# Kernel tuning notes

Measured on AMD Instinct MI355X. Metric: run time of the kernel, lower is better.

Reference implementation:

```python
import jax, jax.numpy as jnp
import numpy as np

EMBED = 256
HEADS = 8
LEVELS = 1
POINTS = 4
NBQ = 2          # num_bev_queue
HBEV = 128
WBEV = 128
BS = 1


def setup_inputs() -> dict:
    key = jax.random.key(0)
    ks = jax.random.split(key, 10)
    Nq = HBEV * WBEV
    E = EMBED
    so_out = NBQ * HEADS * LEVELS * POINTS * 2
    aw_out = NBQ * HEADS * LEVELS * POINTS
    return {
        "query": jax.random.normal(ks[0], (BS, Nq, E), jnp.float32),
        "value": jax.random.normal(ks[1], (BS, NBQ * Nq, E), jnp.float32),
        "reference_points": jax.random.uniform(ks[2], (BS, Nq, LEVELS, 2), jnp.float32),
        # params stored as [in, out]; y = x @ W + b (math-equivalent to torch Linear)
        "W_vproj": jax.random.normal(ks[3], (E, E), jnp.float32) / np.sqrt(E).astype(np.float32),
        "b_vproj": jnp.zeros((E,), jnp.float32),
        "W_so": jax.random.normal(ks[4], (NBQ * E, so_out), jnp.float32) * 0.01,
        "b_so": jax.random.normal(ks[5], (so_out,), jnp.float32) * 0.5,
        "W_aw": jax.random.normal(ks[6], (NBQ * E, aw_out), jnp.float32) * 0.01,
        "b_aw": jnp.zeros((aw_out,), jnp.float32),
        "W_out": jax.random.normal(ks[7], (E, E), jnp.float32) / np.sqrt(E).astype(np.float32),
        "b_out": jnp.zeros((E,), jnp.float32),
        "spatial_shapes": jnp.array([[HBEV, WBEV]], jnp.int32),
        "level_start_index": jnp.array([0], jnp.int32),
    }


def _msda(value, spatial_shapes, sampling_locations, attention_weights):
    """Multi-scale deformable attention (grid_sample semantics: bilinear,
    zero padding, align_corners=False).
    value: [B, sum(H*W), Hh, d]; sampling_locations: [B, Nq, Hh, L, P, 2] in [0,1];
    attention_weights: [B, Nq, Hh, L, P]. Returns [B, Nq, Hh*d]."""
    B, _, Hh, d = value.shape
    _, Nq, _, L, P, _ = sampling_locations.shape
    ss = np.asarray(spatial_shapes)
    out = jnp.zeros((B, Nq, Hh, d), value.dtype)
    start = 0
    for l in range(L):
        H_, W_ = int(ss[l, 0]), int(ss[l, 1])
        v = value[:, start:start + H_ * W_]          # [B, H*W, Hh, d]
        start += H_ * W_
        loc = sampling_locations[:, :, :, l]          # [B, Nq, Hh, P, 2]
        # align_corners=False: pixel = loc*size - 0.5
        px = loc[..., 0] * W_ - 0.5
        py = loc[..., 1] * H_ - 0.5
        x0f = jnp.floor(px)
        y0f = jnp.floor(py)
        lx = px - x0f
        ly = py - y0f
        x0 = x0f.astype(jnp.int32)
        y0 = y0f.astype(jnp.int32)

        def gather(ix, iy):
            valid = ((ix >= 0) & (ix < W_) & (iy >= 0) & (iy < H_))
            idx = jnp.clip(iy, 0, H_ - 1) * W_ + jnp.clip(ix, 0, W_ - 1)   # [B,Nq,Hh,P]
            idx = jnp.transpose(idx, (0, 1, 3, 2)).reshape(B, Nq * P, Hh, 1)
            g = jnp.take_along_axis(v, idx, axis=1).reshape(B, Nq, P, Hh, d)
            m = jnp.transpose(valid, (0, 1, 3, 2))[..., None].astype(value.dtype)
            return g * m

        def wmul(w):  # [B,Nq,Hh,P] -> [B,Nq,P,Hh,1]
            return jnp.transpose(w, (0, 1, 3, 2))[..., None]

        sampled = (wmul((1 - lx) * (1 - ly)) * gather(x0, y0)
                   + wmul(lx * (1 - ly)) * gather(x0 + 1, y0)
                   + wmul((1 - lx) * ly) * gather(x0, y0 + 1)
                   + wmul(lx * ly) * gather(x0 + 1, y0 + 1))   # [B,Nq,P,Hh,d]
        out = out + jnp.einsum('bqphd,bqhp->bqhd', sampled, attention_weights[:, :, :, l])
    return out.reshape(B, Nq, Hh * d)


def reference(query, value, reference_points, W_vproj, b_vproj, W_so, b_so,
              W_aw, b_aw, W_out, b_out, spatial_shapes, level_start_index):
    bs, Nq, E = query.shape
    Hh, L, P, nbq = HEADS, LEVELS, POINTS, NBQ
    identity = query
    # query enhanced with the previous-BEV slice of value
    qe = jnp.concatenate([value[:, :Nq], query], axis=-1)        # [bs, Nq, 2E]
    v = (value @ W_vproj + b_vproj).reshape(bs * nbq, Nq, Hh, E // Hh)
    so = (qe @ W_so + b_so).reshape(bs, Nq, Hh, nbq, L, P, 2)
    aw = jax.nn.softmax((qe @ W_aw + b_aw).reshape(bs, Nq, Hh, nbq, L * P), axis=-1)
    aw = aw.reshape(bs, Nq, Hh, nbq, L, P)
    aw = jnp.transpose(aw, (0, 3, 1, 2, 4, 5)).reshape(bs * nbq, Nq, Hh, L, P)
    so = jnp.transpose(so, (0, 3, 1, 2, 4, 5, 6)).reshape(bs * nbq, Nq, Hh, L, P, 2)
    rp = jnp.tile(reference_points, (nbq, 1, 1, 1))              # [bs*nbq, Nq, L, 2]
    ssf = spatial_shapes.astype(so.dtype)
    offset_normalizer = jnp.stack([ssf[:, 1], ssf[:, 0]], -1)    # [L, 2] = (W, H)
    loc = rp[:, :, None, :, None, :] + so / offset_normalizer[None, None, None, :, None, :]
    out = _msda(v, spatial_shapes, loc, aw).reshape(bs, nbq, Nq, E).mean(axis=1)
    out = out @ W_out + b_out
    return out + identity  # dropout is identity in eval mode
```

## Files before the change

kernel.cpp:

```cpp
#include <hip/hip_runtime.h>
#include <math.h>

#define NQ     16384
#define NHEAD  8
#define GW     128
#define GH     128

typedef __attribute__((ext_vector_type(8))) short short8;
typedef __attribute__((ext_vector_type(4))) float f32x4;

static __device__ __forceinline__ unsigned short f2bf(float f) {
    unsigned u = __builtin_bit_cast(unsigned, f);
    u += 0x7FFFu + ((u >> 16) & 1u);
    return (unsigned short)(u >> 16);
}
static __device__ __forceinline__ unsigned pk2(float lo, float hi) {
    return (unsigned)f2bf(lo) | ((unsigned)f2bf(hi) << 16);
}
static __device__ __forceinline__ float bflo(unsigned u) {
    return __builtin_bit_cast(float, u << 16);
}
static __device__ __forceinline__ float bfhi(unsigned u) {
    return __builtin_bit_cast(float, u & 0xffff0000u);
}

__global__ void prep(const float* __restrict__ Wv, const float* __restrict__ Wso,
                     const float* __restrict__ Waw, const float* __restrict__ bso,
                     const float* __restrict__ baw, const float* __restrict__ Wo,
                     unsigned short* __restrict__ WTv, unsigned short* __restrict__ WTso,
                     unsigned short* __restrict__ WTo, float* __restrict__ bias2)
{
    const int n = blockIdx.x;
    const int k = threadIdx.x;
    WTv[n * 256 + k] = f2bf(Wv[(size_t)k * 256 + n]);
    WTo[n * 256 + k] = f2bf(Wo[(size_t)k * 256 + n]);
    float s0, s1;
    if (n < 128)      { s0 = Wso[(size_t)k * 128 + n];       s1 = Wso[(size_t)(k + 256) * 128 + n]; }
    else if (n < 192) { s0 = Waw[(size_t)k * 64 + n - 128];  s1 = Waw[(size_t)(k + 256) * 64 + n - 128]; }
    else              { s0 = 0.f; s1 = 0.f; }
    WTso[(size_t)n * 512 + k]       = f2bf(s0);
    WTso[(size_t)n * 512 + k + 256] = f2bf(s1);
    if (k == 0) bias2[n] = (n < 128) ? bso[n] : ((n < 192) ? baw[n - 128] : 0.f);
}

template<int KTOT, int MODE>
static __device__ __forceinline__ void gemm_body(
    int m0, int n0,
    const float* __restrict__ A1, const float* __restrict__ A2,
    const unsigned short* __restrict__ Abf,
    const unsigned short* __restrict__ WT,
    const float* __restrict__ bias, const float* __restrict__ resid,
    void* __restrict__ Cout,
    unsigned short* As, unsigned short* Bs)
{
    const int tid = threadIdx.x;
    const int w = tid >> 6, lane = tid & 63;
    const int wr = w >> 1, wc = w & 1;
    const int g = lane >> 4, r16 = lane & 15;

    f32x4 acc[4][4] = {};

    for (int k0 = 0; k0 < KTOT; k0 += 64) {
        if (MODE == 2) {
            #pragma unroll
            for (int c = 0; c < 4; ++c) {
                int idx = tid + c * 256;
                int row = idx >> 3, oct = idx & 7;
                uint4 wv = *reinterpret_cast<const uint4*>(
                    &Abf[(size_t)(m0 + row) * 256 + k0 + oct * 8]);
                *reinterpret_cast<uint4*>(&As[(oct * 128 + row) * 8]) = wv;
            }
        } else {
            const float* Asrc = (KTOT == 512 && k0 >= 256) ? (A2 + (k0 - 256)) : (A1 + k0);
            #pragma unroll
            for (int c = 0; c < 4; ++c) {
                int idx = tid + c * 256;
                int row = idx >> 3, oct = idx & 7;
                const float* p = Asrc + (size_t)(m0 + row) * 256 + oct * 8;
                float4 f0 = *reinterpret_cast<const float4*>(p);
                float4 f1 = *reinterpret_cast<const float4*>(p + 4);
                uint4 wv;
                wv.x = pk2(f0.x, f0.y); wv.y = pk2(f0.z, f0.w);
                wv.z = pk2(f1.x, f1.y); wv.w = pk2(f1.z, f1.w);
                *reinterpret_cast<uint4*>(&As[(oct * 128 + row) * 8]) = wv;
            }
        }
        #pragma unroll
        for (int c = 0; c < 4; ++c) {
            int idx = tid + c * 256;
            int n = idx >> 3, oct = idx & 7;
            uint4 wv = *reinterpret_cast<const uint4*>(
                &WT[(size_t)(n0 + n) * KTOT + k0 + oct * 8]);
            *reinterpret_cast<uint4*>(&Bs[(oct * 128 + n) * 8]) = wv;
        }
        __syncthreads();

        #pragma unroll
        for (int kh = 0; kh < 2; ++kh) {
            short8 af[4], bfr[4];
            #pragma unroll
            for (int m = 0; m < 4; ++m)
                af[m] = *reinterpret_cast<const short8*>(
                    &As[(((kh * 4 + g) * 128) + wr * 64 + m * 16 + r16) * 8]);
            #pragma unroll
            for (int n = 0; n < 4; ++n)
                bfr[n] = *reinterpret_cast<const short8*>(
                    &Bs[(((kh * 4 + g) * 128) + wc * 64 + n * 16 + r16) * 8]);
            #pragma unroll
            for (int m = 0; m < 4; ++m)
                #pragma unroll
                for (int n = 0; n < 4; ++n)
                    acc[m][n] = __builtin_amdgcn_mfma_f32_16x16x32_bf16(
                        af[m], bfr[n], acc[m][n], 0, 0, 0);
        }
        __syncthreads();
    }

    #pragma unroll
    for (int m = 0; m < 4; ++m) {
        int row = m0 + wr * 64 + m * 16 + g * 4;
        #pragma unroll
        for (int n = 0; n < 4; ++n) {
            int col = n0 + wc * 64 + n * 16 + r16;
            if (MODE == 1 && col >= 192) continue;
            float bia = bias[col];
            #pragma unroll
            for (int j = 0; j < 4; ++j) {
                float vo = acc[m][n][j] + bia;
                if (MODE == 0) {
                    ((unsigned short*)Cout)[(size_t)(row + j) * 256 + col] = f2bf(vo);
                } else if (MODE == 1) {
                    ((float*)Cout)[(size_t)(row + j) * 192 + col] = vo;
                } else {
                    ((float*)Cout)[(size_t)(row + j) * 256 + col] =
                        vo + resid[(size_t)(row + j) * 256 + col];
                }
            }
        }
    }
}

__global__ __launch_bounds__(256, 2)
void gemm_vs(const float* __restrict__ value, const float* __restrict__ query,
             const unsigned short* __restrict__ WTv, const unsigned short* __restrict__ WTso,
             const float* __restrict__ bv, const float* __restrict__ bias2,
             unsigned short* __restrict__ v_out, float* __restrict__ soaw_out)
{
    __shared__ __align__(16) unsigned short As[8 * 128 * 8];
    __shared__ __align__(16) unsigned short Bs[8 * 128 * 8];
    const int bid = blockIdx.x;
    if (bid < 512) {
        gemm_body<256, 0>((bid >> 1) * 128, (bid & 1) * 128,
                          value, nullptr, nullptr, WTv, bv, nullptr, v_out, As, Bs);
    } else {
        const int b2 = bid - 512;
        gemm_body<512, 1>((b2 >> 1) * 128, (b2 & 1) * 128,
                          value, query, nullptr, WTso, bias2, nullptr, soaw_out, As, Bs);
    }
}

__global__ __launch_bounds__(256, 2)
void gemm_out(const unsigned short* __restrict__ Abf, const unsigned short* __restrict__ WTo,
              const float* __restrict__ bo, const float* __restrict__ resid,
              float* __restrict__ out)
{
    __shared__ __align__(16) unsigned short As[8 * 128 * 8];
    __shared__ __align__(16) unsigned short Bs[8 * 128 * 8];
    const int bid = blockIdx.x;
    gemm_body<256, 2>((bid >> 1) * 128, (bid & 1) * 128,
                      nullptr, nullptr, Abf, WTo, bo, resid, out, As, Bs);
}

static __device__ __forceinline__ void acc8(float* acc, float w, uint4 r) {
    acc[0] = fmaf(w, bflo(r.x), acc[0]);
    acc[1] = fmaf(w, bfhi(r.x), acc[1]);
    acc[2] = fmaf(w, bflo(r.y), acc[2]);
    acc[3] = fmaf(w, bfhi(r.y), acc[3]);
    acc[4] = fmaf(w, bflo(r.z), acc[4]);
    acc[5] = fmaf(w, bfhi(r.z), acc[5]);
    acc[6] = fmaf(w, bflo(r.w), acc[6]);
    acc[7] = fmaf(w, bfhi(r.w), acc[7]);
}

__global__ __launch_bounds__(256)
void sampler(const unsigned short* __restrict__ v, const float* __restrict__ soaw,
             const float* __restrict__ rp, unsigned short* __restrict__ outm)
{
    __shared__ float so_s[8][128];
    __shared__ float w_s[8][64];
    __shared__ float rp_s[8][2];

    const int t = threadIdx.x;
    const int bid = blockIdx.x;
    const int q0 = ((bid & 7) * 256 + (bid >> 3)) * 8;

    #pragma unroll
    for (int i = 0; i < 4; ++i) {
        int idx = t + i * 256;
        int qq = idx >> 7, off = idx & 127;
        so_s[qq][off] = soaw[(size_t)(q0 + qq) * 192 + off];
    }
    if (t < 128) {
        int qq = t >> 4, grp = t & 15;
        float4 a4 = *reinterpret_cast<const float4*>(
            &soaw[(size_t)(q0 + qq) * 192 + 128 + grp * 4]);
        float m = fmaxf(fmaxf(a4.x, a4.y), fmaxf(a4.z, a4.w));
        float e0 = __expf(a4.x - m), e1 = __expf(a4.y - m);
        float e2 = __expf(a4.z - m), e3 = __expf(a4.w - m);
        float inv = 1.f / (e0 + e1 + e2 + e3);
        w_s[qq][grp * 4 + 0] = e0 * inv;
        w_s[qq][grp * 4 + 1] = e1 * inv;
        w_s[qq][grp * 4 + 2] = e2 * inv;
        w_s[qq][grp * 4 + 3] = e3 * inv;
    }
    if (t < 16) rp_s[t >> 1][t & 1] = rp[(size_t)(q0 + (t >> 1)) * 2 + (t & 1)];
    __syncthreads();

    const int wq = t >> 5;
    const int q = q0 + wq;
    const int s = t & 31;
    const int h = s >> 2, c = s & 3;
    const int sub = h * 64 + c * 16;
    const float rpx = rp_s[wq][0], rpy = rp_s[wq][1];
    float acc[8] = {};

    #pragma unroll
    for (int b = 0; b < 2; ++b) {
        const char* vb = (const char*)v + (size_t)b * NQ * 512;
        #pragma unroll
        for (int p = 0; p < 4; ++p) {
            float sox = so_s[wq][h * 16 + b * 8 + p * 2 + 0];
            float soy = so_s[wq][h * 16 + b * 8 + p * 2 + 1];
            float wbp = w_s[wq][h * 8 + b * 4 + p];
            float px = (rpx + sox * (1.0f / 128.0f)) * 128.0f - 0.5f;
            float py = (rpy + soy * (1.0f / 128.0f)) * 128.0f - 0.5f;
            float x0f = floorf(px), y0f = floorf(py);
            float lx = px - x0f, ly = py - y0f;
            int x0 = (int)x0f, y0 = (int)y0f;
            int x1 = x0 + 1, y1 = y0 + 1;
            float wx0 = (1.f - lx) * ((x0 >= 0 && x0 < GW) ? 1.f : 0.f);
            float wx1 = lx         * ((x1 >= 0 && x1 < GW) ? 1.f : 0.f);
            float wy0 = (1.f - ly) * ((y0 >= 0 && y0 < GH) ? 1.f : 0.f);
            float wy1 = ly         * ((y1 >= 0 && y1 < GH) ? 1.f : 0.f);
            int x0c = min(max(x0, 0), GW - 1), x1c = min(max(x1, 0), GW - 1);
            int y0c = min(max(y0, 0), GH - 1), y1c = min(max(y1, 0), GH - 1);
            uint4 r00 = *(const uint4*)(vb + ((size_t)(y0c * GW + x0c) * 512 + sub));
            uint4 r10 = *(const uint4*)(vb + ((size_t)(y0c * GW + x1c) * 512 + sub));
            uint4 r01 = *(const uint4*)(vb + ((size_t)(y1c * GW + x0c) * 512 + sub));
            uint4 r11 = *(const uint4*)(vb + ((size_t)(y1c * GW + x1c) * 512 + sub));
            acc8(acc, wbp * wx0 * wy0, r00);
            acc8(acc, wbp * wx1 * wy0, r10);
            acc8(acc, wbp * wx0 * wy1, r01);
            acc8(acc, wbp * wx1 * wy1, r11);
        }
    }

    uint4 o;
    o.x = pk2(0.5f * acc[0], 0.5f * acc[1]);
    o.y = pk2(0.5f * acc[2], 0.5f * acc[3]);
    o.z = pk2(0.5f * acc[4], 0.5f * acc[5]);
    o.w = pk2(0.5f * acc[6], 0.5f * acc[7]);
    *reinterpret_cast<uint4*>((char*)outm + (size_t)q * 512 + sub) = o;
}

extern "C" void kernel_launch(void* const* d_in, const int* in_sizes, int n_in,
                              void* d_out, int out_size, void* d_ws, size_t ws_size,
                              hipStream_t stream)
{
    const float* query   = (const float*)d_in[0];
    const float* value   = (const float*)d_in[1];
    const float* rp      = (const float*)d_in[2];
    const float* W_vproj = (const float*)d_in[3];
    const float* b_vproj = (const float*)d_in[4];
    const float* W_so    = (const float*)d_in[5];
    const float* b_so    = (const float*)d_in[6];
    const float* W_aw    = (const float*)d_in[7];
    const float* b_aw    = (const float*)d_in[8];
    const float* W_out   = (const float*)d_in[9];
    const float* b_out   = (const float*)d_in[10];
    float* out = (float*)d_out;

    char* wp = (char*)d_ws;
    unsigned short* ws_v    = (unsigned short*)wp; wp += (size_t)2 * NQ * 256 * 2;
    float*          ws_soaw = (float*)wp;          wp += (size_t)NQ * 192 * 4;
    unsigned short* ws_mean = (unsigned short*)wp; wp += (size_t)NQ * 256 * 2;
    unsigned short* WTv     = (unsigned short*)wp; wp += 256 * 256 * 2;
    unsigned short* WTso    = (unsigned short*)wp; wp += 256 * 512 * 2;
    unsigned short* WTo     = (unsigned short*)wp; wp += 256 * 256 * 2;
    float*          bias2   = (float*)wp;          wp += 256 * 4;

    prep<<<dim3(256), dim3(256), 0, stream>>>(W_vproj, W_so, W_aw, b_so, b_aw, W_out,
                                              WTv, WTso, WTo, bias2);
    gemm_vs<<<dim3(768), dim3(256), 0, stream>>>(value, query, WTv, WTso,
                                                 b_vproj, bias2, ws_v, ws_soaw);
    sampler<<<dim3(NQ / 8), dim3(256), 0, stream>>>(ws_v, ws_soaw, rp, ws_mean);
    gemm_out<<<dim3(256), dim3(256), 0, stream>>>(ws_mean, WTo, b_out, query, out);
}
```

Baseline: 95.53 us.

## Pad GEMM LDS tiles, remap block roles, split sampler queues across half-waves

The GEMM shared-memory tiles get a padded stride (1032 instead of 1024 per k-octet) to reduce LDS bank conflicts on the MFMA fragment loads. Block indices are remapped so consecutive blocks share row tiles differently, aiming at better cache locality. The sampler now uses a 64-lane wave per query, with each half-wave handling one BEV queue and combining results by a cross-lane shuffle. This doubles parallelism and the number of sampler blocks. It adds a shuffle and leaves half the lanes idle during the store.

```diff
diff --git a/kernel.cpp b/kernel.cpp
--- a/kernel.cpp
+++ b/kernel.cpp
@@ -43,6 +43,8 @@
     if (k == 0) bias2[n] = (n < 128) ? bso[n] : ((n < 192) ? baw[n - 128] : 0.f);
 }
 
+#define PL(oct, row) ((oct) * 1032 + (row) * 8)
+
 template<int KTOT, int MODE>
 static __device__ __forceinline__ void gemm_body(
     int m0, int n0,
@@ -68,7 +70,7 @@
                 int row = idx >> 3, oct = idx & 7;
                 uint4 wv = *reinterpret_cast<const uint4*>(
                     &Abf[(size_t)(m0 + row) * 256 + k0 + oct * 8]);
-                *reinterpret_cast<uint4*>(&As[(oct * 128 + row) * 8]) = wv;
+                *reinterpret_cast<uint4*>(&As[PL(oct, row)]) = wv;
             }
         } else {
             const float* Asrc = (KTOT == 512 && k0 >= 256) ? (A2 + (k0 - 256)) : (A1 + k0);
@@ -82,7 +84,7 @@
                 uint4 wv;
                 wv.x = pk2(f0.x, f0.y); wv.y = pk2(f0.z, f0.w);
                 wv.z = pk2(f1.x, f1.y); wv.w = pk2(f1.z, f1.w);
-                *reinterpret_cast<uint4*>(&As[(oct * 128 + row) * 8]) = wv;
+                *reinterpret_cast<uint4*>(&As[PL(oct, row)]) = wv;
             }
         }
         #pragma unroll
@@ -91,7 +93,7 @@
             int n = idx >> 3, oct = idx & 7;
             uint4 wv = *reinterpret_cast<const uint4*>(
                 &WT[(size_t)(n0 + n) * KTOT + k0 + oct * 8]);
-            *reinterpret_cast<uint4*>(&Bs[(oct * 128 + n) * 8]) = wv;
+            *reinterpret_cast<uint4*>(&Bs[PL(oct, n)]) = wv;
         }
         __syncthreads();
 
@@ -101,11 +103,11 @@
             #pragma unroll
             for (int m = 0; m < 4; ++m)
                 af[m] = *reinterpret_cast<const short8*>(
-                    &As[(((kh * 4 + g) * 128) + wr * 64 + m * 16 + r16) * 8]);
+                    &As[PL(kh * 4 + g, wr * 64 + m * 16 + r16)]);
             #pragma unroll
             for (int n = 0; n < 4; ++n)
                 bfr[n] = *reinterpret_cast<const short8*>(
-                    &Bs[(((kh * 4 + g) * 128) + wc * 64 + n * 16 + r16) * 8]);
+                    &Bs[PL(kh * 4 + g, wc * 64 + n * 16 + r16)]);
             #pragma unroll
             for (int m = 0; m < 4; ++m)
                 #pragma unroll
@@ -146,15 +148,17 @@
              const float* __restrict__ bv, const float* __restrict__ bias2,
              unsigned short* __restrict__ v_out, float* __restrict__ soaw_out)
 {
-    __shared__ __align__(16) unsigned short As[8 * 128 * 8];
-    __shared__ __align__(16) unsigned short Bs[8 * 128 * 8];
-    const int bid = blockIdx.x;
-    if (bid < 512) {
-        gemm_body<256, 0>((bid >> 1) * 128, (bid & 1) * 128,
+    __shared__ __align__(16) unsigned short As[8 * 1032];
+    __shared__ __align__(16) unsigned short Bs[8 * 1032];
+    const int b = blockIdx.x;
+    if (b < 512) {
+        const int role = ((b >> 4) * 8 + (b & 7)) * 2 + ((b >> 3) & 1);
+        gemm_body<256, 0>((role >> 1) * 128, (role & 1) * 128,
                           value, nullptr, nullptr, WTv, bv, nullptr, v_out, As, Bs);
     } else {
-        const int b2 = bid - 512;
-        gemm_body<512, 1>((b2 >> 1) * 128, (b2 & 1) * 128,
+        const int j = b - 512;
+        const int role = ((j >> 4) * 8 + (j & 7)) * 2 + ((j >> 3) & 1);
+        gemm_body<512, 1>((role >> 1) * 128, (role & 1) * 128,
                           value, query, nullptr, WTso, bias2, nullptr, soaw_out, As, Bs);
     }
 }
@@ -164,10 +168,11 @@
               const float* __restrict__ bo, const float* __restrict__ resid,
               float* __restrict__ out)
 {
-    __shared__ __align__(16) unsigned short As[8 * 128 * 8];
-    __shared__ __align__(16) unsigned short Bs[8 * 128 * 8];
-    const int bid = blockIdx.x;
-    gemm_body<256, 2>((bid >> 1) * 128, (bid & 1) * 128,
+    __shared__ __align__(16) unsigned short As[8 * 1032];
+    __shared__ __align__(16) unsigned short Bs[8 * 1032];
+    const int b = blockIdx.x;
+    const int role = ((b >> 4) * 8 + (b & 7)) * 2 + ((b >> 3) & 1);
+    gemm_body<256, 2>((role >> 1) * 128, (role & 1) * 128,
                       nullptr, nullptr, Abf, WTo, bo, resid, out, As, Bs);
 }
 
@@ -186,21 +191,21 @@
 void sampler(const unsigned short* __restrict__ v, const float* __restrict__ soaw,
              const float* __restrict__ rp, unsigned short* __restrict__ outm)
 {
-    __shared__ float so_s[8][128];
-    __shared__ float w_s[8][64];
-    __shared__ float rp_s[8][2];
+    __shared__ float so_s[4][128];
+    __shared__ float w_s[4][64];
+    __shared__ float rp_s[4][2];
 
     const int t = threadIdx.x;
     const int bid = blockIdx.x;
-    const int q0 = ((bid & 7) * 256 + (bid >> 3)) * 8;
+    const int q0 = ((bid & 7) * 512 + (bid >> 3)) * 4;
 
     #pragma unroll
-    for (int i = 0; i < 4; ++i) {
+    for (int i = 0; i < 2; ++i) {
         int idx = t + i * 256;
         int qq = idx >> 7, off = idx & 127;
         so_s[qq][off] = soaw[(size_t)(q0 + qq) * 192 + off];
     }
-    if (t < 128) {
+    if (t < 64) {
         int qq = t >> 4, grp = t & 15;
         float4 a4 = *reinterpret_cast<const float4*>(
             &soaw[(size_t)(q0 + qq) * 192 + 128 + grp * 4]);
@@ -213,54 +218,58 @@
         w_s[qq][grp * 4 + 2] = e2 * inv;
         w_s[qq][grp * 4 + 3] = e3 * inv;
     }
-    if (t < 16) rp_s[t >> 1][t & 1] = rp[(size_t)(q0 + (t >> 1)) * 2 + (t & 1)];
+    if (t < 8) rp_s[t >> 1][t & 1] = rp[(size_t)(q0 + (t >> 1)) * 2 + (t & 1)];
     __syncthreads();
 
-    const int wq = t >> 5;
+    const int wq = t >> 6;
     const int q = q0 + wq;
-    const int s = t & 31;
+    const int ln = t & 63;
+    const int b = ln >> 5;
+    const int s = ln & 31;
     const int h = s >> 2, c = s & 3;
     const int sub = h * 64 + c * 16;
     const float rpx = rp_s[wq][0], rpy = rp_s[wq][1];
+    const char* vb = (const char*)v + (size_t)b * NQ * 512;
     float acc[8] = {};
 
     #pragma unroll
-    for (int b = 0; b < 2; ++b) {
-        const char* vb = (const char*)v + (size_t)b * NQ * 512;
-        #pragma unroll
-        for (int p = 0; p < 4; ++p) {
-            float sox = so_s[wq][h * 16 + b * 8 + p * 2 + 0];
-            float soy = so_s[wq][h * 16 + b * 8 + p * 2 + 1];
-            float wbp = w_s[wq][h * 8 + b * 4 + p];
-            float px = (rpx + sox * (1.0f / 128.0f)) * 128.0f - 0.5f;
-            float py = (rpy + soy * (1.0f / 128.0f)) * 128.0f - 0.5f;
-            float x0f = floorf(px), y0f = floorf(py);
-            float lx = px - x0f, ly = py - y0f;
-            int x0 = (int)x0f, y0 = (int)y0f;
-            int x1 = x0 + 1, y1 = y0 + 1;
-            float wx0 = (1.f - lx) * ((x0 >= 0 && x0 < GW) ? 1.f : 0.f);
-            float wx1 = lx         * ((x1 >= 0 && x1 < GW) ? 1.f : 0.f);
-            float wy0 = (1.f - ly) * ((y0 >= 0 && y0 < GH) ? 1.f : 0.f);
-            float wy1 = ly         * ((y1 >= 0 && y1 < GH) ? 1.f : 0.f);
-            int x0c = min(max(x0, 0), GW - 1), x1c = min(max(x1, 0), GW - 1);
-            int y0c = min(max(y0, 0), GH - 1), y1c = min(max(y1, 0), GH - 1);
-            uint4 r00 = *(const uint4*)(vb + ((size_t)(y0c * GW + x0c) * 512 + sub));
-            uint4 r10 = *(const uint4*)(vb + ((size_t)(y0c * GW + x1c) * 512 + sub));
-            uint4 r01 = *(const uint4*)(vb + ((size_t)(y1c * GW + x0c) * 512 + sub));
-            uint4 r11 = *(const uint4*)(vb + ((size_t)(y1c * GW + x1c) * 512 + sub));
-            acc8(acc, wbp * wx0 * wy0, r00);
-            acc8(acc, wbp * wx1 * wy0, r10);
-            acc8(acc, wbp * wx0 * wy1, r01);
-            acc8(acc, wbp * wx1 * wy1, r11);
-        }
-    }
-
-    uint4 o;
-    o.x = pk2(0.5f * acc[0], 0.5f * acc[1]);
-    o.y = pk2(0.5f * acc[2], 0.5f * acc[3]);
-    o.z = pk2(0.5f * acc[4], 0.5f * acc[5]);
-    o.w = pk2(0.5f * acc[6], 0.5f * acc[7]);
-    *reinterpret_cast<uint4*>((char*)outm + (size_t)q * 512 + sub) = o;
+    for (int p = 0; p < 4; ++p) {
+        float sox = so_s[wq][h * 16 + b * 8 + p * 2 + 0];
+        float soy = so_s[wq][h * 16 + b * 8 + p * 2 + 1];
+        float wbp = w_s[wq][h * 8 + b * 4 + p];
+        float px = (rpx + sox * (1.0f / 128.0f)) * 128.0f - 0.5f;
+        float py = (rpy + soy * (1.0f / 128.0f)) * 128.0f - 0.5f;
+        float x0f = floorf(px), y0f = floorf(py);
+        float lx = px - x0f, ly = py - y0f;
+        int x0 = (int)x0f, y0 = (int)y0f;
+        int x1 = x0 + 1, y1 = y0 + 1;
+        float wx0 = (1.f - lx) * ((x0 >= 0 && x0 < GW) ? 1.f : 0.f);
+        float wx1 = lx         * ((x1 >= 0 && x1 < GW) ? 1.f : 0.f);
+        float wy0 = (1.f - ly) * ((y0 >= 0 && y0 < GH) ? 1.f : 0.f);
+        float wy1 = ly         * ((y1 >= 0 && y1 < GH) ? 1.f : 0.f);
+        int x0c = min(max(x0, 0), GW - 1), x1c = min(max(x1, 0), GW - 1);
+        int y0c = min(max(y0, 0), GH - 1), y1c = min(max(y1, 0), GH - 1);
+        uint4 r00 = *(const uint4*)(vb + ((size_t)(y0c * GW + x0c) * 512 + sub));
+        uint4 r10 = *(const uint4*)(vb + ((size_t)(y0c * GW + x1c) * 512 + sub));
+        uint4 r01 = *(const uint4*)(vb + ((size_t)(y1c * GW + x0c) * 512 + sub));
+        uint4 r11 = *(const uint4*)(vb + ((size_t)(y1c * GW + x1c) * 512 + sub));
+        acc8(acc, wbp * wx0 * wy0, r00);
+        acc8(acc, wbp * wx1 * wy0, r10);
+        acc8(acc, wbp * wx0 * wy1, r01);
+        acc8(acc, wbp * wx1 * wy1, r11);
+    }
+
+    #pragma unroll
+    for (int i = 0; i < 8; ++i) acc[i] += __shfl_xor(acc[i], 32);
+
+    if (b == 0) {
+        uint4 o;
+        o.x = pk2(0.5f * acc[0], 0.5f * acc[1]);
+        o.y = pk2(0.5f * acc[2], 0.5f * acc[3]);
+        o.z = pk2(0.5f * acc[4], 0.5f * acc[5]);
+        o.w = pk2(0.5f * acc[6], 0.5f * acc[7]);
+        *reinterpret_cast<uint4*>((char*)outm + (size_t)q * 512 + sub) = o;
+    }
 }
 
 extern "C" void kernel_launch(void* const* d_in, const int* in_sizes, int n_in,
@@ -293,6 +302,6 @@
                                               WTv, WTso, WTo, bias2);
     gemm_vs<<<dim3(768), dim3(256), 0, stream>>>(value, query, WTv, WTso,
                                                  b_vproj, bias2, ws_v, ws_soaw);
-    sampler<<<dim3(NQ / 8), dim3(256), 0, stream>>>(ws_v, ws_soaw, rp, ws_mean);
+    sampler<<<dim3(NQ / 4), dim3(256), 0, stream>>>(ws_v, ws_soaw, rp, ws_mean);
     gemm_out<<<dim3(256), dim3(256), 0, stream>>>(ws_mean, WTo, b_out, query, out);
 }
```

Result: faster. 92.46 us (-3.2%).
